# Performance work log

Measured on AMD Instinct MI355X. Metric: run time of the kernel, lower is better.

The kernel has to match this reference:

```python
import jax, jax.numpy as jnp
import numpy as np

LN_EPS = 1e-5


def setup_inputs() -> dict:
    key = jax.random.key(0)
    k1, k2, k3 = jax.random.split(key, 3)
    B, K, S, H, D = 8, 32, 4096, 2048, 1024
    plan_embeddings = jax.random.normal(k1, (B, S, H), dtype=jnp.float32)
    ownership = jax.random.bernoulli(k2, 0.5, (B, K, S))  # bool (B, K, S)
    W = jax.random.normal(k3, (H, D), dtype=jnp.float32) * (1.0 / np.sqrt(H))
    b = jnp.zeros((D,), dtype=jnp.float32)
    gamma = jnp.ones((D,), dtype=jnp.float32)
    beta = jnp.zeros((D,), dtype=jnp.float32)
    return {
        "plan_embeddings": plan_embeddings,
        "ownership": ownership,
        "W": W,
        "b": b,
        "gamma": gamma,
        "beta": beta,
    }


def reference(plan_embeddings, ownership, W, b, gamma, beta):
    # ownership-weighted mean pooling over slots S (same math as the
    # broadcast-multiply + sum in the torch original, expressed as an einsum
    # so no (B,K,S,H) intermediate is materialized)
    own_f = ownership.astype(plan_embeddings.dtype)          # (B, K, S)
    summed = jnp.einsum('bks,bsh->bkh', own_f, plan_embeddings)  # (B, K, H)
    counts = jnp.clip(own_f.sum(axis=-1, keepdims=True), 1.0)   # (B, K, 1)
    pooled = summed / counts                                   # (B, K, H)
    # linear projection
    projected = pooled @ W + b                                 # (B, K, D)
    # LayerNorm over last dim
    mu = projected.mean(axis=-1, keepdims=True)
    var = jnp.mean(jnp.square(projected - mu), axis=-1, keepdims=True)
    normed = (projected - mu) * jax.lax.rsqrt(var + LN_EPS)
    return normed * gamma + beta
```

## Files before the change

### kernel.cpp

```cpp
#include <hip/hip_runtime.h>

typedef unsigned int u32;
typedef unsigned short u16;
typedef __attribute__((ext_vector_type(8))) short short8;
typedef __attribute__((ext_vector_type(4))) float f32x4;
typedef __attribute__((ext_vector_type(16))) float f32x16;

#define BB 8
#define KK 32
#define SS 4096
#define HH 2048
#define DD 1024
#define NSC 8
#define SC_S 512

#define OFF_W16  0ull
#define OFF_WB   (2ull << 20)
#define OFF_PART (6ull << 20)
#define OFF_PQ   (22ull << 20)
#define OFF_PROJ (23ull << 20)

__device__ __forceinline__ u16 f2bf(float x) {
  u32 u = __float_as_uint(x);
  return (u16)((u + 0x7fffu + ((u >> 16) & 1u)) >> 16);
}

__global__ __launch_bounds__(256) void k_prep(const void* __restrict__ own,
                                              u16* __restrict__ w16,
                                              const float* __restrict__ W,
                                              u16* __restrict__ WB) {
  __shared__ float lds[64][65];
  const int t = threadIdx.x;

  if (blockIdx.x < BB * KK) {
    const int bk = blockIdx.x;
    __shared__ int s_mode;
    __shared__ int s_wcnt[4];
    __shared__ float s_inv;

    if (t < 64) {
      u32 w = ((const u32*)own)[t];
      bool wordok = (w <= 1u) || (w == 0x3f800000u);
      unsigned long long m = __ballot(wordok);
      if (t == 0) s_mode = (m == ~0ull) ? 1 : 0;
    }
    __syncthreads();
    const int mode = s_mode;

    u32 bits = 0;
    const size_t base = (size_t)bk * SS + (size_t)t * 16;
    if (mode == 0) {
      uint4 v = *(const uint4*)((const unsigned char*)own + base);
      u32 wa[4] = {v.x, v.y, v.z, v.w};
#pragma unroll
      for (int w = 0; w < 4; ++w)
#pragma unroll
        for (int j = 0; j < 4; ++j)
          if ((wa[w] >> (8 * j)) & 0xffu) bits |= 1u << (4 * w + j);
    } else {
      const u32* p = (const u32*)own + base;
#pragma unroll
      for (int j = 0; j < 16; ++j)
        if (p[j] != 0u) bits |= 1u << j;
    }

    int cnt = __popc(bits);
#pragma unroll
    for (int off = 1; off < 64; off <<= 1) cnt += __shfl_xor(cnt, off);
    if ((t & 63) == 0) s_wcnt[t >> 6] = cnt;
    __syncthreads();
    if (t == 0) {
      int tot = s_wcnt[0] + s_wcnt[1] + s_wcnt[2] + s_wcnt[3];
      s_inv = 1.0f / fmaxf((float)tot, 1.0f);
    }
    __syncthreads();
    const u32 hv = (u32)f2bf(s_inv);

    u32 outw[8];
#pragma unroll
    for (int j = 0; j < 8; ++j) {
      u32 lo = ((bits >> (2 * j)) & 1u) ? hv : 0u;
      u32 hi = ((bits >> (2 * j + 1)) & 1u) ? hv : 0u;
      outw[j] = lo | (hi << 16);
    }
    u32* wo = (u32*)w16 + (size_t)bk * (SS / 2) + (size_t)t * 8;
    uint4 o0 = {outw[0], outw[1], outw[2], outw[3]};
    uint4 o1 = {outw[4], outw[5], outw[6], outw[7]};
    ((uint4*)wo)[0] = o0;
    ((uint4*)wo)[1] = o1;
  } else {
    const int bidx = blockIdx.x - BB * KK;
    const int hb = (bidx & 31) * 64, db = (bidx >> 5) * 64;
    const int x = t & 63, y = t >> 6;
#pragma unroll
    for (int j = 0; j < 16; ++j) {
      int r = y + 4 * j;
      lds[r][x] = W[(size_t)(hb + r) * DD + db + x];
    }
    __syncthreads();
#pragma unroll
    for (int j = 0; j < 16; ++j) {
      int r = y + 4 * j;
      WB[(size_t)(db + r) * HH + hb + x] = f2bf(lds[x][r]);
    }
  }
}

__global__ __launch_bounds__(1024, 4) void k_pool(const float* __restrict__ plan,
                                                  const u16* __restrict__ w16,
                                                  float* __restrict__ part) {
  const int hcb = blockIdx.x, sc = blockIdx.y, b = blockIdx.z;
  const int t = threadIdx.x, w = t >> 6, l = t & 63;
  const int lc = l & 31, half = l >> 5;
  const int h0 = hcb * 512 + w * 32;
  const int s0 = sc * SC_S;

  const float* pb = plan + (size_t)b * SS * HH + h0 + lc;
  const u16* wa = w16 + (size_t)(b * KK + lc) * SS;

  f32x16 acc;
#pragma unroll
  for (int r = 0; r < 16; ++r) acc[r] = 0.0f;

  for (int step = 0; step < 32; ++step) {
    const int sb = s0 + step * 16 + half * 8;
    short8 a = *(const short8*)(wa + sb);
    const float* col = pb + (size_t)sb * HH;
    float f[8];
#pragma unroll
    for (int j = 0; j < 8; ++j) f[j] = col[(size_t)j * HH];
    short8 bfr;
#pragma unroll
    for (int j = 0; j < 8; ++j) bfr[j] = (short)f2bf(f[j]);
    acc = __builtin_amdgcn_mfma_f32_32x32x16_bf16(a, bfr, acc, 0, 0, 0);
  }

  float* po = part + ((size_t)sc * BB + b) * KK * HH + h0 + lc;
#pragma unroll
  for (int r = 0; r < 16; ++r) {
    int krow = (r & 3) + 8 * (r >> 2) + 4 * half;
    po[(size_t)krow * HH] = acc[r];
  }
}

__global__ __launch_bounds__(256) void k_reduce(const float* __restrict__ part,
                                                u32* __restrict__ pq) {
  const int i = blockIdx.x * 256 + threadIdx.x;
  const int row = i >> 10, hp = i & 1023;
  const float* p = part + (size_t)row * HH + 2 * hp;
  float lo = 0.f, hi = 0.f;
#pragma unroll
  for (int sc = 0; sc < NSC; ++sc) {
    float2 v = *(const float2*)(p + (size_t)sc * BB * KK * HH);
    lo += v.x;
    hi += v.y;
  }
  pq[i] = (u32)f2bf(lo) | ((u32)f2bf(hi) << 16);
}

__global__ __launch_bounds__(256) void k_proj(const u16* __restrict__ pq,
                                              const u16* __restrict__ WB,
                                              const float* __restrict__ bias,
                                              float* __restrict__ proj) {
  const int rt = blockIdx.x, ctg = blockIdx.y;
  const int t = threadIdx.x, w = t >> 6, l = t & 63;
  const int lr = l & 15, lg = l >> 4;
  const int r0 = rt * 16, c0 = (ctg * 4 + w) * 16;

  const u16* pa = pq + (size_t)(r0 + lr) * HH + lg * 8;
  const u16* pw = WB + (size_t)(c0 + lr) * HH + lg * 8;
  f32x4 acc = (f32x4){0.f, 0.f, 0.f, 0.f};
#pragma unroll 4
  for (int slab = 0; slab < 64; ++slab) {
    short8 a = *(const short8*)(pa + slab * 32);
    short8 bv = *(const short8*)(pw + slab * 32);
    acc = __builtin_amdgcn_mfma_f32_16x16x32_bf16(a, bv, acc, 0, 0, 0);
  }
  const float bs = bias[c0 + lr];
#pragma unroll
  for (int j = 0; j < 4; ++j)
    proj[(size_t)(r0 + lg * 4 + j) * DD + c0 + lr] = acc[j] + bs;
}

__global__ __launch_bounds__(256) void k_ln(const float* __restrict__ proj,
                                            const float* __restrict__ gamma,
                                            const float* __restrict__ beta,
                                            float* __restrict__ out) {
  const int row = blockIdx.x, t = threadIdx.x;
  float4 v = ((const float4*)(proj + (size_t)row * DD))[t];
  float s1 = v.x + v.y + v.z + v.w;
  float s2 = v.x * v.x + v.y * v.y + v.z * v.z + v.w * v.w;
#pragma unroll
  for (int off = 1; off < 64; off <<= 1) {
    s1 += __shfl_xor(s1, off);
    s2 += __shfl_xor(s2, off);
  }
  __shared__ float a1[4], a2[4];
  if ((t & 63) == 0) { a1[t >> 6] = s1; a2[t >> 6] = s2; }
  __syncthreads();
  const float S1 = a1[0] + a1[1] + a1[2] + a1[3];
  const float S2 = a2[0] + a2[1] + a2[2] + a2[3];
  const float mu = S1 * (1.0f / DD);
  const float var = S2 * (1.0f / DD) - mu * mu;
  const float rs = rsqrtf(var + 1e-5f);
  float4 g = ((const float4*)gamma)[t];
  float4 be = ((const float4*)beta)[t];
  float4 o;
  o.x = (v.x - mu) * rs * g.x + be.x;
  o.y = (v.y - mu) * rs * g.y + be.y;
  o.z = (v.z - mu) * rs * g.z + be.z;
  o.w = (v.w - mu) * rs * g.w + be.w;
  ((float4*)(out + (size_t)row * DD))[t] = o;
}


extern "C" void kernel_launch(void* const* d_in, const int* in_sizes, int n_in,
                              void* d_out, int out_size, void* d_ws, size_t ws_size,
                              hipStream_t stream) {
  (void)in_sizes; (void)n_in; (void)out_size; (void)ws_size;
  const float* plan  = (const float*)d_in[0];
  const void*  own   = d_in[1];
  const float* W     = (const float*)d_in[2];
  const float* bias  = (const float*)d_in[3];
  const float* gamma = (const float*)d_in[4];
  const float* beta  = (const float*)d_in[5];
  float* out = (float*)d_out;
  char* ws = (char*)d_ws;

  u16*   w16  = (u16*)(ws + OFF_W16);
  u16*   WB   = (u16*)(ws + OFF_WB);
  float* part = (float*)(ws + OFF_PART);
  u32*   pq   = (u32*)(ws + OFF_PQ);
  float* proj = (float*)(ws + OFF_PROJ);

  k_prep<<<dim3(BB * KK + (HH / 64) * (DD / 64)), dim3(256), 0, stream>>>(own, w16, W, WB);
  k_pool<<<dim3(HH / 512, NSC, BB), dim3(1024), 0, stream>>>(plan, w16, part);
  k_reduce<<<dim3((BB * KK * (HH / 2)) / 256), dim3(256), 0, stream>>>(part, pq);
  k_proj<<<dim3(16, 16), dim3(256), 0, stream>>>((const u16*)pq, WB, bias, proj);
  k_ln<<<dim3(BB * KK), dim3(256), 0, stream>>>(proj, gamma, beta, out);
}
```

Baseline: 85.30 us.

## Replace split-S partial buffer and reduce kernel with atomic accumulation

After: 87.22 us. 1.02x slower.

```diff
diff --git a/kernel.cpp b/kernel.cpp
--- a/kernel.cpp
+++ b/kernel.cpp
@@ -11,14 +11,13 @@
 #define SS 4096
 #define HH 2048
 #define DD 1024
-#define NSC 8
-#define SC_S 512
-
-#define OFF_W16  0ull
-#define OFF_WB   (2ull << 20)
-#define OFF_PART (6ull << 20)
-#define OFF_PQ   (22ull << 20)
-#define OFF_PROJ (23ull << 20)
+#define NSC 16
+#define SC_S 256
+
+#define OFF_W16    0ull
+#define OFF_WB     (2ull << 20)
+#define OFF_POOLED (6ull << 20)
+#define OFF_PROJ   (8ull << 20)
 
 __device__ __forceinline__ u16 f2bf(float x) {
   u32 u = __float_as_uint(x);
@@ -28,9 +27,15 @@
 __global__ __launch_bounds__(256) void k_prep(const void* __restrict__ own,
                                               u16* __restrict__ w16,
                                               const float* __restrict__ W,
-                                              u16* __restrict__ WB) {
+                                              u16* __restrict__ WB,
+                                              float* __restrict__ pooled) {
   __shared__ float lds[64][65];
   const int t = threadIdx.x;
+
+  if (blockIdx.x < 512) {
+    f32x4 z = (f32x4){0.f, 0.f, 0.f, 0.f};
+    ((f32x4*)pooled)[(size_t)blockIdx.x * 256 + t] = z;
+  }
 
   if (blockIdx.x < BB * KK) {
     const int bk = blockIdx.x;
@@ -106,9 +111,9 @@
   }
 }
 
-__global__ __launch_bounds__(1024, 4) void k_pool(const float* __restrict__ plan,
+__global__ __launch_bounds__(1024, 8) void k_pool(const float* __restrict__ plan,
                                                   const u16* __restrict__ w16,
-                                                  float* __restrict__ part) {
+                                                  float* __restrict__ pooled) {
   const int hcb = blockIdx.x, sc = blockIdx.y, b = blockIdx.z;
   const int t = threadIdx.x, w = t >> 6, l = t & 63;
   const int lc = l & 31, half = l >> 5;
@@ -122,7 +127,7 @@
 #pragma unroll
   for (int r = 0; r < 16; ++r) acc[r] = 0.0f;
 
-  for (int step = 0; step < 32; ++step) {
+  for (int step = 0; step < SC_S / 16; ++step) {
     const int sb = s0 + step * 16 + half * 8;
     short8 a = *(const short8*)(wa + sb);
     const float* col = pb + (size_t)sb * HH;
@@ -135,30 +140,15 @@
     acc = __builtin_amdgcn_mfma_f32_32x32x16_bf16(a, bfr, acc, 0, 0, 0);
   }
 
-  float* po = part + ((size_t)sc * BB + b) * KK * HH + h0 + lc;
+  float* po = pooled + (size_t)(b * KK) * HH + h0 + lc;
 #pragma unroll
   for (int r = 0; r < 16; ++r) {
     int krow = (r & 3) + 8 * (r >> 2) + 4 * half;
-    po[(size_t)krow * HH] = acc[r];
-  }
-}
-
-__global__ __launch_bounds__(256) void k_reduce(const float* __restrict__ part,
-                                                u32* __restrict__ pq) {
-  const int i = blockIdx.x * 256 + threadIdx.x;
-  const int row = i >> 10, hp = i & 1023;
-  const float* p = part + (size_t)row * HH + 2 * hp;
-  float lo = 0.f, hi = 0.f;
-#pragma unroll
-  for (int sc = 0; sc < NSC; ++sc) {
-    float2 v = *(const float2*)(p + (size_t)sc * BB * KK * HH);
-    lo += v.x;
-    hi += v.y;
-  }
-  pq[i] = (u32)f2bf(lo) | ((u32)f2bf(hi) << 16);
-}
-
-__global__ __launch_bounds__(256) void k_proj(const u16* __restrict__ pq,
+    atomicAdd(&po[(size_t)krow * HH], acc[r]);
+  }
+}
+
+__global__ __launch_bounds__(256) void k_proj(const float* __restrict__ pooled,
                                               const u16* __restrict__ WB,
                                               const float* __restrict__ bias,
                                               float* __restrict__ proj) {
@@ -167,12 +157,19 @@
   const int lr = l & 15, lg = l >> 4;
   const int r0 = rt * 16, c0 = (ctg * 4 + w) * 16;
 
-  const u16* pa = pq + (size_t)(r0 + lr) * HH + lg * 8;
+  const float* pa = pooled + (size_t)(r0 + lr) * HH + lg * 8;
   const u16* pw = WB + (size_t)(c0 + lr) * HH + lg * 8;
   f32x4 acc = (f32x4){0.f, 0.f, 0.f, 0.f};
 #pragma unroll 4
   for (int slab = 0; slab < 64; ++slab) {
-    short8 a = *(const short8*)(pa + slab * 32);
+    f32x4 x0 = *(const f32x4*)(pa + slab * 32);
+    f32x4 x1 = *(const f32x4*)(pa + slab * 32 + 4);
+    short8 a;
+#pragma unroll
+    for (int j = 0; j < 4; ++j) {
+      a[j] = (short)f2bf(x0[j]);
+      a[j + 4] = (short)f2bf(x1[j]);
+    }
     short8 bv = *(const short8*)(pw + slab * 32);
     acc = __builtin_amdgcn_mfma_f32_16x16x32_bf16(a, bv, acc, 0, 0, 0);
   }
@@ -227,15 +224,13 @@
   float* out = (float*)d_out;
   char* ws = (char*)d_ws;
 
-  u16*   w16  = (u16*)(ws + OFF_W16);
-  u16*   WB   = (u16*)(ws + OFF_WB);
-  float* part = (float*)(ws + OFF_PART);
-  u32*   pq   = (u32*)(ws + OFF_PQ);
-  float* proj = (float*)(ws + OFF_PROJ);
-
-  k_prep<<<dim3(BB * KK + (HH / 64) * (DD / 64)), dim3(256), 0, stream>>>(own, w16, W, WB);
-  k_pool<<<dim3(HH / 512, NSC, BB), dim3(1024), 0, stream>>>(plan, w16, part);
-  k_reduce<<<dim3((BB * KK * (HH / 2)) / 256), dim3(256), 0, stream>>>(part, pq);
-  k_proj<<<dim3(16, 16), dim3(256), 0, stream>>>((const u16*)pq, WB, bias, proj);
+  u16*   w16    = (u16*)(ws + OFF_W16);
+  u16*   WB     = (u16*)(ws + OFF_WB);
+  float* pooled = (float*)(ws + OFF_POOLED);
+  float* proj   = (float*)(ws + OFF_PROJ);
+
+  k_prep<<<dim3(BB * KK + (HH / 64) * (DD / 64)), dim3(256), 0, stream>>>(own, w16, W, WB, pooled);
+  k_pool<<<dim3(HH / 512, NSC, BB), dim3(1024), 0, stream>>>(plan, w16, pooled);
+  k_proj<<<dim3(16, 16), dim3(256), 0, stream>>>(pooled, WB, bias, proj);
   k_ln<<<dim3(BB * KK), dim3(256), 0, stream>>>(proj, gamma, beta, out);
 }
```
